# Kernel optimization log

Measured on AMD Instinct MI355X. Metric: run time of the kernel, lower is better.

Reference implementation:

```python
import jax, jax.numpy as jnp
import numpy as np


def _gcn_norm(edge_index, edge_weight, n_nodes):
    # PyG gcn_norm with add_self_loops=True, fill_value=1.0.
    row, col = edge_index[0], edge_index[1]
    loop = jnp.arange(n_nodes, dtype=edge_index.dtype)
    row = jnp.concatenate([row, loop])
    col = jnp.concatenate([col, loop])
    w = jnp.concatenate([edge_weight, jnp.ones((n_nodes,), edge_weight.dtype)])
    deg = jax.ops.segment_sum(w, col, num_segments=n_nodes)
    dinv = jnp.where(deg > 0, jax.lax.rsqrt(deg), 0.0)
    norm = dinv[row] * w * dinv[col]
    return row, col, norm


def _gcn_conv(x, row, col, norm, W, b, n_nodes):
    h = x @ W                                  # [N, F_out]
    msg = h[row] * norm[:, None]               # gather + scale, [E+N, F_out]
    out = jax.ops.segment_sum(msg, col, num_segments=n_nodes)
    return out + b


def setup_inputs() -> dict:
    key = jax.random.key(0)
    k = jax.random.split(key, 7)
    N, E, Fin, Fout = 50000, 1600000, 256, 128
    H = 2 * Fout
    x = jax.random.normal(k[0], (N, Fin), dtype=jnp.float32)
    edge_index = jax.random.randint(k[1], (2, E), 0, N, dtype=jnp.int64)
    edge_weight = jax.random.uniform(k[2], (E,), dtype=jnp.float32)
    # Glorot init as in PyG GCNConv (weight stored as [in, out] here)
    s1 = float(np.sqrt(6.0 / (Fin + H)))
    s2 = float(np.sqrt(6.0 / (H + Fout)))
    W1 = jax.random.uniform(k[3], (Fin, H), minval=-s1, maxval=s1, dtype=jnp.float32)
    b1 = jnp.zeros((H,), jnp.float32)
    W2 = jax.random.uniform(k[4], (H, Fout), minval=-s2, maxval=s2, dtype=jnp.float32)
    b2 = jnp.zeros((Fout,), jnp.float32)
    return {"x": x, "edge_index": edge_index, "edge_weight": edge_weight,
            "W1": W1, "b1": b1, "W2": W2, "b2": b2}


def reference(x, edge_index, edge_weight, W1, b1, W2, b2):
    n_nodes = x.shape[0]
    # cached=True: normalization computed once, reused by both layers
    row, col, norm = _gcn_norm(edge_index, edge_weight, n_nodes)
    h = _gcn_conv(x, row, col, norm, W1, b1, n_nodes)
    h = jax.nn.relu(h)
    out = _gcn_conv(h, row, col, norm, W2, b2, n_nodes)
    return out
```

## Files before the change

### kernel.cpp

```cpp
#include <hip/hip_runtime.h>

typedef __attribute__((ext_vector_type(8))) short  short8;
typedef __attribute__((ext_vector_type(4))) float  f32x4;
typedef __attribute__((ext_vector_type(4))) ushort us4;
typedef __attribute__((ext_vector_type(4))) uint   u32x4;
typedef __attribute__((ext_vector_type(2))) uint   u32x2;

__device__ __forceinline__ float bf2f(ushort u) {
    union { uint i; float f; } c; c.i = ((uint)u) << 16; return c.f;
}
__device__ __forceinline__ float bits2f(uint b) {
    union { uint i; float f; } c; c.i = b; return c.f;
}
__device__ __forceinline__ ushort f2bf(float f) {
    union { float f; uint i; } c; c.f = f;
    uint b = c.i + 0x7fffu + ((c.i >> 16) & 1u);
    return (ushort)(b >> 16);
}

#define CMAX  96
#define NBLK  256
#define NBMAX 1024

__global__ void k_histA(const int* __restrict__ col, int* __restrict__ counts,
                        int E, int NB) {
    __shared__ uint hist[NBMAX];
    for (int j = threadIdx.x; j < NB; j += 256) hist[j] = 0u;
    __syncthreads();
    for (int i = blockIdx.x * 256 + threadIdx.x; i < E; i += 256 * NBLK)
        atomicAdd(&hist[((uint)col[i]) >> 6], 1u);
    __syncthreads();
    for (int j = threadIdx.x; j < NB; j += 256)
        counts[j * NBLK + blockIdx.x] = (int)hist[j];
}

__global__ void k_scanB1(int* __restrict__ counts, int* __restrict__ btot) {
    __shared__ int s[256];
    int b = blockIdx.x, t = threadIdx.x;
    int v = counts[b * NBLK + t];
    s[t] = v; __syncthreads();
    for (int off = 1; off < 256; off <<= 1) {
        int x = (t >= off) ? s[t - off] : 0;
        __syncthreads();
        s[t] += x;
        __syncthreads();
    }
    counts[b * NBLK + t] = s[t] - v;
    if (t == 255) btot[b] = s[255];
}

__global__ void k_scanB2(const int* __restrict__ btot, int* __restrict__ bbase, int NB) {
    __shared__ int s[256];
    int t = threadIdx.x;
    int v[4]; int sum = 0;
    #pragma unroll
    for (int j = 0; j < 4; ++j) {
        int i = t * 4 + j;
        v[j] = (i < NB) ? btot[i] : 0;
        sum += v[j];
    }
    s[t] = sum; __syncthreads();
    for (int off = 1; off < 256; off <<= 1) {
        int x = (t >= off) ? s[t - off] : 0;
        __syncthreads();
        s[t] += x;
        __syncthreads();
    }
    int excl = s[t] - sum;
    #pragma unroll
    for (int j = 0; j < 4; ++j) {
        int i = t * 4 + j;
        if (i <= NB) bbase[i] = excl;
        excl += v[j];
    }
}

__global__ void k_binC(const int* __restrict__ row, const int* __restrict__ col,
                       const float* __restrict__ w,
                       const int* __restrict__ counts, const int* __restrict__ bbase,
                       unsigned long long* __restrict__ recs, int E, int NB) {
    __shared__ uint cur[NBMAX];
    for (int j = threadIdx.x; j < NB; j += 256)
        cur[j] = (uint)(bbase[j] + counts[j * NBLK + blockIdx.x]);
    __syncthreads();
    for (int i = blockIdx.x * 256 + threadIdx.x; i < E; i += 256 * NBLK) {
        int c = col[i], r = row[i];
        float wv = w[i];
        uint w16 = (uint)(wv * 65536.0f);
        if (w16 > 65535u) w16 = 65535u;
        uint b = ((uint)c) >> 6;
        uint pos = atomicAdd(&cur[b], 1u);
        recs[pos] = ((unsigned long long)(uint)c << 32)
                  | (unsigned long long)((w16 << 16) | (uint)(r & 0xffff));
    }
}

__global__ void k_binD(const unsigned long long* __restrict__ recs,
                       const int* __restrict__ bbase,
                       uint* __restrict__ edgesP, int* __restrict__ cntp,
                       float* __restrict__ dinv, int N, int NB) {
    __shared__ uint cnt[64], ws[64], cur2[64];
    int b = blockIdx.x, t = threadIdx.x;
    if (t < 64) { cnt[t] = 0u; ws[t] = 0u; cur2[t] = 0u; }
    __syncthreads();
    int lo = bbase[b], hi = bbase[b + 1];
    for (int i = lo + t; i < hi; i += 256) {
        unsigned long long rec = recs[i];
        uint cl = ((uint)(rec >> 32)) & 63u;
        atomicAdd(&cnt[cl], 1u);
        atomicAdd(&ws[cl], (uint)((rec >> 16) & 0xffffu));
    }
    __syncthreads();
    for (int i = lo + t; i < hi; i += 256) {
        unsigned long long rec = recs[i];
        uint cg = (uint)(rec >> 32);
        uint slot = atomicAdd(&cur2[cg & 63u], 1u);
        if (slot < CMAX) edgesP[(size_t)cg * CMAX + slot] = (uint)rec;
    }
    __syncthreads();
    if (t < 64) {
        int node = b * 64 + t;
        if (node < N) {
            uint c0 = cnt[t];
            if (c0 > CMAX) c0 = CMAX;
            int cp = (int)((c0 + 3u) & ~3u);
            for (int j = (int)c0; j < cp; ++j)
                edgesP[(size_t)node * CMAX + j] = 0u;
            float deg = 1.0f + (float)ws[t] * (1.0f / 65536.0f);
            dinv[node] = rsqrtf(deg);
            cntp[node] = cp;
        }
    }
}

__global__ void k_splitT(const float* __restrict__ W, ushort* __restrict__ Th,
                         ushort* __restrict__ Tl, int K, int N) {
    int i = blockIdx.x * 256 + threadIdx.x;
    if (i < K * N) {
        int k = i / N, n = i - k * N;
        float v = W[i];
        ushort hi = f2bf(v);
        ushort lo = f2bf(v - bf2f(hi));
        Th[(size_t)n * K + k] = hi;
        Tl[(size_t)n * K + k] = lo;
    }
}

#define LDA 40

__global__ __launch_bounds__(256)
void k_gemm3(const float* __restrict__ A, const ushort* __restrict__ BTh,
             const ushort* __restrict__ BTl, ushort* __restrict__ Cpan,
             const float* __restrict__ dinv, int M, int Nc, int K) {
    __shared__ __align__(16) ushort As[2][128][LDA];
    __shared__ __align__(16) ushort Bs[2][128][LDA];

    const int t    = threadIdx.x;
    const int lane = t & 63;
    const int wid  = t >> 6;
    const int wm   = wid >> 1;
    const int wn   = wid & 1;
    const int ml   = lane & 15;
    const int kq   = lane >> 4;
    const int bm   = blockIdx.y * 128;
    const int bn   = blockIdx.x * 128;

    f32x4 acc[4][4];
    #pragma unroll
    for (int mt = 0; mt < 4; ++mt)
        #pragma unroll
        for (int nt = 0; nt < 4; ++nt) acc[mt][nt] = (f32x4){0.f, 0.f, 0.f, 0.f};

    for (int k0 = 0; k0 < K; k0 += 32) {
        #pragma unroll
        for (int it = 0; it < 4; ++it) {
            int idx = (t + it * 256) * 4;
            int r  = idx >> 5;
            int kk = idx & 31;
            int grow = bm + r;
            f32x4 v = (f32x4){0.f, 0.f, 0.f, 0.f};
            if (grow < M) v = *(const f32x4*)&A[(size_t)grow * K + k0 + kk];
            us4 hi, lo;
            #pragma unroll
            for (int j = 0; j < 4; ++j) {
                ushort h = f2bf(v[j]);
                hi[j] = h;
                lo[j] = f2bf(v[j] - bf2f(h));
            }
            *(us4*)&As[0][r][kk] = hi;
            *(us4*)&As[1][r][kk] = lo;
        }
        #pragma unroll
        for (int it = 0; it < 2; ++it) {
            int idx = (t + it * 256) * 8;
            int n  = idx >> 5;
            int kk = idx & 31;
            u32x4 vh = *(const u32x4*)&BTh[(size_t)(bn + n) * K + k0 + kk];
            *(u32x4*)&Bs[0][n][kk] = vh;
            u32x4 vl = *(const u32x4*)&BTl[(size_t)(bn + n) * K + k0 + kk];
            *(u32x4*)&Bs[1][n][kk] = vl;
        }
        __syncthreads();

        short8 a[4][2], b[4][2];
        #pragma unroll
        for (int mt = 0; mt < 4; ++mt) {
            a[mt][0] = *(const short8*)&As[0][wm * 64 + mt * 16 + ml][kq * 8];
            a[mt][1] = *(const short8*)&As[1][wm * 64 + mt * 16 + ml][kq * 8];
        }
        #pragma unroll
        for (int nt = 0; nt < 4; ++nt) {
            b[nt][0] = *(const short8*)&Bs[0][wn * 64 + nt * 16 + ml][kq * 8];
            b[nt][1] = *(const short8*)&Bs[1][wn * 64 + nt * 16 + ml][kq * 8];
        }
        #pragma unroll
        for (int mt = 0; mt < 4; ++mt)
            #pragma unroll
            for (int nt = 0; nt < 4; ++nt) {
                acc[mt][nt] = __builtin_amdgcn_mfma_f32_16x16x32_bf16(a[mt][0], b[nt][0], acc[mt][nt], 0, 0, 0);
                acc[mt][nt] = __builtin_amdgcn_mfma_f32_16x16x32_bf16(a[mt][0], b[nt][1], acc[mt][nt], 0, 0, 0);
                acc[mt][nt] = __builtin_amdgcn_mfma_f32_16x16x32_bf16(a[mt][1], b[nt][0], acc[mt][nt], 0, 0, 0);
            }
        __syncthreads();
    }

    #pragma unroll
    for (int mt = 0; mt < 4; ++mt) {
        int rbase = bm + wm * 64 + mt * 16 + kq * 4;
        #pragma unroll
        for (int nt = 0; nt < 4; ++nt) {
            int colg = bn + wn * 64 + nt * 16 + ml;
            size_t pbase = (size_t)(colg >> 5) * M * 32 + (colg & 31);
            #pragma unroll
            for (int r = 0; r < 4; ++r) {
                int rr = rbase + r;
                if (rr < M) Cpan[pbase + (size_t)rr * 32] = f2bf(acc[mt][nt][r] * dinv[rr]);
            }
        }
    }
}

#define NODES_PER_BLK 32

template <bool RELU>
__device__ __forceinline__
void aggr_body(const int* __restrict__ cntp, const uint* __restrict__ edges,
               const ushort* __restrict__ hpan, const float* __restrict__ dinv,
               const float* __restrict__ bias, float* __restrict__ out,
               int F, int npan, int N) {
    const int bid  = blockIdx.x;
    const int p    = bid % npan;
    const int wave = threadIdx.x >> 6;
    const int lane = threadIdx.x & 63;
    const int g    = lane >> 3;
    const int c    = lane & 7;
    const int node = (bid / npan) * NODES_PER_BLK + wave * 8 + g;
    const int fbase = p * 32 + c * 4;

    const ushort* hp = hpan + (size_t)p * N * 32 + c * 4;

    int beg = 0, end = 0;
    if (node < N) { beg = node * CMAX; end = beg + cntp[node]; }

    float a0 = 0.f, a1 = 0.f, a2 = 0.f, a3 = 0.f;
    int e = beg;
    u32x4 pk4 = (u32x4){0u, 0u, 0u, 0u};
    if (e < end) pk4 = *(const u32x4*)&edges[e];
    while (__any(e < end)) {
        u32x4 cur = pk4;
        int e2 = e + 4;
        if (e2 < end) pk4 = *(const u32x4*)&edges[e2];
        if (e < end) {
            #pragma unroll
            for (int j = 0; j < 4; ++j) {
                uint pk = cur[j];
                float nv = (float)(pk >> 16);
                int r = (int)(pk & 0xffffu);
                u32x2 hv = *(const u32x2*)(hp + (size_t)r * 32);
                a0 += nv * bits2f(hv[0] << 16);
                a1 += nv * bits2f(hv[0] & 0xffff0000u);
                a2 += nv * bits2f(hv[1] << 16);
                a3 += nv * bits2f(hv[1] & 0xffff0000u);
            }
        }
        e = e2;
    }

    if (node < N) {
        float dc = dinv[node];
        float sc = dc * (1.0f / 65536.0f);
        u32x2 hs = *(const u32x2*)(hp + (size_t)node * 32);
        f32x4 bv = *(const f32x4*)&bias[fbase];
        f32x4 v;
        v[0] = fmaf(sc, a0, fmaf(dc, bits2f(hs[0] << 16),         bv[0]));
        v[1] = fmaf(sc, a1, fmaf(dc, bits2f(hs[0] & 0xffff0000u), bv[1]));
        v[2] = fmaf(sc, a2, fmaf(dc, bits2f(hs[1] << 16),         bv[2]));
        v[3] = fmaf(sc, a3, fmaf(dc, bits2f(hs[1] & 0xffff0000u), bv[3]));
        if (RELU) {
            v[0] = fmaxf(v[0], 0.f); v[1] = fmaxf(v[1], 0.f);
            v[2] = fmaxf(v[2], 0.f); v[3] = fmaxf(v[3], 0.f);
        }
        *(f32x4*)&out[(size_t)node * F + fbase] = v;
    }
}

__global__ __launch_bounds__(256)
void k_aggr1(const int* __restrict__ cntp, const uint* __restrict__ edges,
             const ushort* __restrict__ hpan, const float* __restrict__ dinv,
             const float* __restrict__ bias, float* __restrict__ out,
             int F, int npan, int N) {
    aggr_body<true>(cntp, edges, hpan, dinv, bias, out, F, npan, N);
}

__global__ __launch_bounds__(256)
void k_aggr2(const int* __restrict__ cntp, const uint* __restrict__ edges,
             const ushort* __restrict__ hpan, const float* __restrict__ dinv,
             const float* __restrict__ bias, float* __restrict__ out,
             int F, int npan, int N) {
    aggr_body<false>(cntp, edges, hpan, dinv, bias, out, F, npan, N);
}


static inline char* bump(char*& p, size_t bytes) {
    char* r = p;
    p += (bytes + 255) & ~(size_t)255;
    return r;
}

extern "C" void kernel_launch(void* const* d_in, const int* in_sizes, int n_in,
                              void* d_out, int out_size, void* d_ws, size_t ws_size,
                              hipStream_t stream) {
    const float* x  = (const float*)d_in[0];
    const int*   ei = (const int*)d_in[1];
    const float* ew = (const float*)d_in[2];
    const float* W1 = (const float*)d_in[3];
    const float* b1 = (const float*)d_in[4];
    const float* W2 = (const float*)d_in[5];
    const float* b2 = (const float*)d_in[6];
    float* out = (float*)d_out;

    const int E    = in_sizes[2];
    const int H    = in_sizes[4];
    const int Fout = in_sizes[6];
    const int Fin  = in_sizes[3] / H;
    const int N    = in_sizes[0] / Fin;
    const int NB   = (N + 63) >> 6;

    const int* row = ei;
    const int* col = ei + E;

    char* p = (char*)d_ws;
    float*  dinv   = (float*)bump(p, (size_t)N * 4);
    int*    cntp   = (int*)bump(p, (size_t)N * 4);
    uint*   edgesP = (uint*)bump(p, (size_t)N * CMAX * 4);
    int*    counts = (int*)bump(p, (size_t)NBMAX * NBLK * 4);
    int*    btot   = (int*)bump(p, (size_t)NBMAX * 4);
    int*    bbase  = (int*)bump(p, (size_t)(NBMAX + 1) * 4);
    ushort* WT1h   = (ushort*)bump(p, (size_t)Fin * H * 2);
    ushort* WT1l   = (ushort*)bump(p, (size_t)Fin * H * 2);
    ushort* WT2h   = (ushort*)bump(p, (size_t)H * Fout * 2);
    ushort* WT2l   = (ushort*)bump(p, (size_t)H * Fout * 2);
    ushort* h1     = (ushort*)bump(p, (size_t)N * H * 2);
    float*  a1     = (float*)bump(p, (size_t)N * H * 4);
    ushort* h2     = (ushort*)bump(p, (size_t)N * Fout * 2);

    unsigned long long* recs = (unsigned long long*)a1;

    k_splitT<<<(Fin * H + 255) / 256, 256, 0, stream>>>(W1, WT1h, WT1l, Fin, H);
    k_splitT<<<(H * Fout + 255) / 256, 256, 0, stream>>>(W2, WT2h, WT2l, H, Fout);

    k_histA<<<NBLK, 256, 0, stream>>>(col, counts, E, NB);
    k_scanB1<<<NB, 256, 0, stream>>>(counts, btot);
    k_scanB2<<<1, 256, 0, stream>>>(btot, bbase, NB);
    k_binC<<<NBLK, 256, 0, stream>>>(row, col, ew, counts, bbase, recs, E, NB);
    k_binD<<<NB, 256, 0, stream>>>(recs, bbase, edgesP, cntp, dinv, N, NB);

    const int chunks = (N + NODES_PER_BLK - 1) / NODES_PER_BLK;

    k_gemm3<<<dim3(H / 128, (N + 127) / 128), 256, 0, stream>>>(x, WT1h, WT1l, h1, dinv, N, H, Fin);
    k_aggr1<<<chunks * (H / 32), 256, 0, stream>>>(cntp, edgesP, h1, dinv, b1, a1, H, H / 32, N);

    k_gemm3<<<dim3(Fout / 128, (N + 127) / 128), 256, 0, stream>>>(a1, WT2h, WT2l, h2, dinv, N, Fout, H);
    k_aggr2<<<chunks * (Fout / 32), 256, 0, stream>>>(cntp, edgesP, h2, dinv, b2, out, Fout, Fout / 32, N);
}
```

Baseline: 419.6 us.

## Overlap graph binning with layer-1 GEMM and switch to compact CSR with precomputed norms

Fuses the histogram and weight-split kernels into one launch. The edge binning and degree stages now share launches with slices of the layer-1 GEMM so that graph preprocessing overlaps matrix work, which is possible because the GEMM no longer scales its output by dinv. Edges move from a fixed CMAX=96 slot-per-node layout to a compact CSR with per-bin prefix sums, and each edge stores its full normalized weight in bf16, so aggregation no longer applies dinv. This adds an extra scan and pass, removes the degree truncation at CMAX, and lowers precision of the edge norm to bf16.

```diff
diff --git a/kernel.cpp b/kernel.cpp
--- a/kernel.cpp
+++ b/kernel.cpp
@@ -5,6 +5,7 @@
 typedef __attribute__((ext_vector_type(4))) ushort us4;
 typedef __attribute__((ext_vector_type(4))) uint   u32x4;
 typedef __attribute__((ext_vector_type(2))) uint   u32x2;
+typedef unsigned long long ull;
 
 __device__ __forceinline__ float bf2f(ushort u) {
     union { uint i; float f; } c; c.i = ((uint)u) << 16; return c.f;
@@ -18,13 +19,12 @@
     return (ushort)(b >> 16);
 }
 
-#define CMAX  96
 #define NBLK  256
 #define NBMAX 1024
 
-__global__ void k_histA(const int* __restrict__ col, int* __restrict__ counts,
-                        int E, int NB) {
-    __shared__ uint hist[NBMAX];
+__device__ __forceinline__
+void histA_body(const int* __restrict__ col, int* __restrict__ counts,
+                int E, int NB, uint* hist) {
     for (int j = threadIdx.x; j < NB; j += 256) hist[j] = 0u;
     __syncthreads();
     for (int i = blockIdx.x * 256 + threadIdx.x; i < E; i += 256 * NBLK)
@@ -32,6 +32,102 @@
     __syncthreads();
     for (int j = threadIdx.x; j < NB; j += 256)
         counts[j * NBLK + blockIdx.x] = (int)hist[j];
+}
+
+__device__ __forceinline__
+void binC_body(const int* __restrict__ row, const int* __restrict__ col,
+               const float* __restrict__ w,
+               const int* __restrict__ counts, const int* __restrict__ bbase,
+               ull* __restrict__ recs, int E, int NB, uint* cur) {
+    for (int j = threadIdx.x; j < NB; j += 256)
+        cur[j] = (uint)(bbase[j] + counts[j * NBLK + blockIdx.x]);
+    __syncthreads();
+    for (int i = blockIdx.x * 256 + threadIdx.x; i < E; i += 256 * NBLK) {
+        int c = col[i], r = row[i];
+        float wv = w[i];
+        uint w16 = (uint)(wv * 65536.0f);
+        if (w16 > 65535u) w16 = 65535u;
+        uint pos = atomicAdd(&cur[((uint)c) >> 6], 1u);
+        recs[pos] = ((ull)(uint)c << 32) | (ull)((w16 << 16) | (uint)(r & 0xffff));
+    }
+}
+
+__device__ __forceinline__
+void binDa_body(const ull* __restrict__ recs, const int* __restrict__ bbase,
+                int* __restrict__ cntp, float* __restrict__ dinv,
+                int* __restrict__ btotP, int N,
+                uint* cnt, uint* ws, uint* red) {
+    int b = blockIdx.x, t = threadIdx.x;
+    if (t < 64) { cnt[t] = 0u; ws[t] = 0u; }
+    __syncthreads();
+    int lo = bbase[b], hi = bbase[b + 1];
+    for (int i = lo + t; i < hi; i += 256) {
+        ull rec = recs[i];
+        atomicAdd(&cnt[((uint)(rec >> 32)) & 63u], 1u);
+        atomicAdd(&ws[((uint)(rec >> 32)) & 63u], (uint)((rec >> 16) & 0xffffu));
+    }
+    __syncthreads();
+    uint cp = 0;
+    if (t < 64) {
+        int node = b * 64 + t;
+        if (node < N) {
+            cp = (cnt[t] + 3u) & ~3u;
+            cntp[node] = (int)cp;
+            dinv[node] = rsqrtf(1.0f + (float)ws[t] * (1.0f / 65536.0f));
+        }
+        red[t] = cp;
+    }
+    __syncthreads();
+    if (t < 32) red[t] += red[t + 32];
+    __syncthreads();
+    if (t < 16) red[t] += red[t + 16];
+    __syncthreads();
+    if (t < 8) red[t] += red[t + 8];
+    __syncthreads();
+    if (t < 4) red[t] += red[t + 4];
+    __syncthreads();
+    if (t == 0) btotP[b] = (int)(red[0] + red[1] + red[2] + red[3]);
+}
+
+__device__ __forceinline__
+void binDb_body(const ull* __restrict__ recs, const int* __restrict__ bbase,
+                const int* __restrict__ bbaseP, const int* __restrict__ cntp,
+                const float* __restrict__ dinv, int* __restrict__ rowptr,
+                uint* __restrict__ edgesP, int N,
+                uint* arr, uint* curN, uint* rbs) {
+    int b = blockIdx.x, t = threadIdx.x;
+    int node = b * 64 + t;
+    uint cp = 0;
+    if (t < 64 && node < N) cp = (uint)cntp[node];
+    if (t < 64) arr[t] = cp;
+    __syncthreads();
+    for (int off = 1; off < 64; off <<= 1) {
+        uint x = (t < 64 && t >= off) ? arr[t - off] : 0u;
+        __syncthreads();
+        if (t < 64) arr[t] += x;
+        __syncthreads();
+    }
+    if (t < 64) {
+        uint rb = (uint)bbaseP[b] + arr[t] - cp;
+        rbs[t] = rb; curN[t] = rb;
+        if (node < N) rowptr[node] = (int)rb;
+    }
+    __syncthreads();
+    int lo = bbase[b], hi = bbase[b + 1];
+    for (int i = lo + t; i < hi; i += 256) {
+        ull rec = recs[i];
+        uint c   = (uint)(rec >> 32);
+        uint r   = (uint)rec & 0xffffu;
+        uint w16 = ((uint)rec >> 16) & 0xffffu;
+        float nv = dinv[r] * ((float)w16 * (1.0f / 65536.0f)) * dinv[c];
+        uint slot = atomicAdd(&curN[c & 63u], 1u);
+        edgesP[slot] = r | ((uint)f2bf(nv) << 16);
+    }
+    __syncthreads();
+    if (t < 64 && node < N) {
+        uint e1 = rbs[t] + cp;
+        for (uint j = curN[t]; j < e1; ++j) edgesP[j] = 0u;
+    }
 }
 
 __global__ void k_scanB1(int* __restrict__ counts, int* __restrict__ btot) {
@@ -75,67 +171,9 @@
     }
 }
 
-__global__ void k_binC(const int* __restrict__ row, const int* __restrict__ col,
-                       const float* __restrict__ w,
-                       const int* __restrict__ counts, const int* __restrict__ bbase,
-                       unsigned long long* __restrict__ recs, int E, int NB) {
-    __shared__ uint cur[NBMAX];
-    for (int j = threadIdx.x; j < NB; j += 256)
-        cur[j] = (uint)(bbase[j] + counts[j * NBLK + blockIdx.x]);
-    __syncthreads();
-    for (int i = blockIdx.x * 256 + threadIdx.x; i < E; i += 256 * NBLK) {
-        int c = col[i], r = row[i];
-        float wv = w[i];
-        uint w16 = (uint)(wv * 65536.0f);
-        if (w16 > 65535u) w16 = 65535u;
-        uint b = ((uint)c) >> 6;
-        uint pos = atomicAdd(&cur[b], 1u);
-        recs[pos] = ((unsigned long long)(uint)c << 32)
-                  | (unsigned long long)((w16 << 16) | (uint)(r & 0xffff));
-    }
-}
-
-__global__ void k_binD(const unsigned long long* __restrict__ recs,
-                       const int* __restrict__ bbase,
-                       uint* __restrict__ edgesP, int* __restrict__ cntp,
-                       float* __restrict__ dinv, int N, int NB) {
-    __shared__ uint cnt[64], ws[64], cur2[64];
-    int b = blockIdx.x, t = threadIdx.x;
-    if (t < 64) { cnt[t] = 0u; ws[t] = 0u; cur2[t] = 0u; }
-    __syncthreads();
-    int lo = bbase[b], hi = bbase[b + 1];
-    for (int i = lo + t; i < hi; i += 256) {
-        unsigned long long rec = recs[i];
-        uint cl = ((uint)(rec >> 32)) & 63u;
-        atomicAdd(&cnt[cl], 1u);
-        atomicAdd(&ws[cl], (uint)((rec >> 16) & 0xffffu));
-    }
-    __syncthreads();
-    for (int i = lo + t; i < hi; i += 256) {
-        unsigned long long rec = recs[i];
-        uint cg = (uint)(rec >> 32);
-        uint slot = atomicAdd(&cur2[cg & 63u], 1u);
-        if (slot < CMAX) edgesP[(size_t)cg * CMAX + slot] = (uint)rec;
-    }
-    __syncthreads();
-    if (t < 64) {
-        int node = b * 64 + t;
-        if (node < N) {
-            uint c0 = cnt[t];
-            if (c0 > CMAX) c0 = CMAX;
-            int cp = (int)((c0 + 3u) & ~3u);
-            for (int j = (int)c0; j < cp; ++j)
-                edgesP[(size_t)node * CMAX + j] = 0u;
-            float deg = 1.0f + (float)ws[t] * (1.0f / 65536.0f);
-            dinv[node] = rsqrtf(deg);
-            cntp[node] = cp;
-        }
-    }
-}
-
-__global__ void k_splitT(const float* __restrict__ W, ushort* __restrict__ Th,
-                         ushort* __restrict__ Tl, int K, int N) {
-    int i = blockIdx.x * 256 + threadIdx.x;
+__device__ __forceinline__
+void splitT_body(const float* __restrict__ W, ushort* __restrict__ Th,
+                 ushort* __restrict__ Tl, int K, int N, int i) {
     if (i < K * N) {
         int k = i / N, n = i - k * N;
         float v = W[i];
@@ -148,13 +186,11 @@
 
 #define LDA 40
 
-__global__ __launch_bounds__(256)
-void k_gemm3(const float* __restrict__ A, const ushort* __restrict__ BTh,
-             const ushort* __restrict__ BTl, ushort* __restrict__ Cpan,
-             const float* __restrict__ dinv, int M, int Nc, int K) {
-    __shared__ __align__(16) ushort As[2][128][LDA];
-    __shared__ __align__(16) ushort Bs[2][128][LDA];
-
+__device__ __forceinline__
+void gemm3_body(const float* __restrict__ A, const ushort* __restrict__ BTh,
+                const ushort* __restrict__ BTl, ushort* __restrict__ Cpan,
+                int M, int Nc, int K, int bm, int bn,
+                ushort (*As)[128][LDA], ushort (*Bs)[128][LDA]) {
     const int t    = threadIdx.x;
     const int lane = t & 63;
     const int wid  = t >> 6;
@@ -162,8 +198,6 @@
     const int wn   = wid & 1;
     const int ml   = lane & 15;
     const int kq   = lane >> 4;
-    const int bm   = blockIdx.y * 128;
-    const int bn   = blockIdx.x * 128;
 
     f32x4 acc[4][4];
     #pragma unroll
@@ -234,17 +268,97 @@
             #pragma unroll
             for (int r = 0; r < 4; ++r) {
                 int rr = rbase + r;
-                if (rr < M) Cpan[pbase + (size_t)rr * 32] = f2bf(acc[mt][nt][r] * dinv[rr]);
+                if (rr < M) Cpan[pbase + (size_t)rr * 32] = f2bf(acc[mt][nt][r]);
             }
         }
     }
 }
 
+__global__ __launch_bounds__(256)
+void k_gemm3(const float* __restrict__ A, const ushort* __restrict__ BTh,
+             const ushort* __restrict__ BTl, ushort* __restrict__ Cpan,
+             int M, int Nc, int K) {
+    __shared__ __align__(16) ushort As[2][128][LDA];
+    __shared__ __align__(16) ushort Bs[2][128][LDA];
+    gemm3_body(A, BTh, BTl, Cpan, M, Nc, K, blockIdx.y * 128, blockIdx.x * 128, As, Bs);
+}
+
+__global__ __launch_bounds__(256)
+void k_fusedA(const int* __restrict__ col, int* __restrict__ counts, int E, int NB,
+              const float* __restrict__ W1, ushort* __restrict__ WT1h, ushort* __restrict__ WT1l,
+              int Fin, int H,
+              const float* __restrict__ W2, ushort* __restrict__ WT2h, ushort* __restrict__ WT2l,
+              int Fout, int sp1) {
+    __shared__ uint hist[NBMAX];
+    int bid = (int)blockIdx.x;
+    if (bid < NBLK) { histA_body(col, counts, E, NB, hist); return; }
+    if (bid < NBLK + sp1) { splitT_body(W1, WT1h, WT1l, Fin, H, (bid - NBLK) * 256 + (int)threadIdx.x); return; }
+    splitT_body(W2, WT2h, WT2l, H, Fout, (bid - NBLK - sp1) * 256 + (int)threadIdx.x);
+}
+
+__global__ __launch_bounds__(256)
+void k_fusedB1(const int* __restrict__ row, const int* __restrict__ col,
+               const float* __restrict__ w, const int* __restrict__ counts,
+               const int* __restrict__ bbase, ull* __restrict__ recs, int E, int NB,
+               const float* __restrict__ A, const ushort* __restrict__ BTh,
+               const ushort* __restrict__ BTl, ushort* __restrict__ Cpan,
+               int M, int Nc, int K, int t0) {
+    __shared__ __align__(16) ushort As[2][128][LDA];
+    __shared__ __align__(16) ushort Bs[2][128][LDA];
+    int bid = (int)blockIdx.x;
+    if (bid < NBLK) { binC_body(row, col, w, counts, bbase, recs, E, NB, (uint*)&As[0][0][0]); return; }
+    int tile = t0 + bid - NBLK;
+    int nbn = Nc >> 7;
+    gemm3_body(A, BTh, BTl, Cpan, M, Nc, K, (tile / nbn) * 128, (tile % nbn) * 128, As, Bs);
+}
+
+__global__ __launch_bounds__(256)
+void k_fusedB2(const ull* __restrict__ recs, const int* __restrict__ bbase,
+               int* __restrict__ cntp, float* __restrict__ dinv, int* __restrict__ btotP,
+               int N, int NB,
+               const float* __restrict__ A, const ushort* __restrict__ BTh,
+               const ushort* __restrict__ BTl, ushort* __restrict__ Cpan,
+               int M, int Nc, int K, int t0) {
+    __shared__ __align__(16) ushort As[2][128][LDA];
+    __shared__ __align__(16) ushort Bs[2][128][LDA];
+    int bid = (int)blockIdx.x;
+    if (bid < NB) {
+        uint* l = (uint*)&As[0][0][0];
+        binDa_body(recs, bbase, cntp, dinv, btotP, N, l, l + 64, l + 128);
+        return;
+    }
+    int tile = t0 + bid - NB;
+    int nbn = Nc >> 7;
+    gemm3_body(A, BTh, BTl, Cpan, M, Nc, K, (tile / nbn) * 128, (tile % nbn) * 128, As, Bs);
+}
+
+__global__ __launch_bounds__(256)
+void k_fusedB3(const ull* __restrict__ recs, const int* __restrict__ bbase,
+               const int* __restrict__ bbaseP, const int* __restrict__ cntp,
+               const float* __restrict__ dinv, int* __restrict__ rowptr,
+               uint* __restrict__ edgesP, int N, int NB,
+               const float* __restrict__ A, const ushort* __restrict__ BTh,
+               const ushort* __restrict__ BTl, ushort* __restrict__ Cpan,
+               int M, int Nc, int K, int t0) {
+    __shared__ __align__(16) ushort As[2][128][LDA];
+    __shared__ __align__(16) ushort Bs[2][128][LDA];
+    int bid = (int)blockIdx.x;
+    if (bid < NB) {
+        uint* l = (uint*)&As[0][0][0];
+        binDb_body(recs, bbase, bbaseP, cntp, dinv, rowptr, edgesP, N, l, l + 64, l + 128);
+        return;
+    }
+    int tile = t0 + bid - NB;
+    int nbn = Nc >> 7;
+    gemm3_body(A, BTh, BTl, Cpan, M, Nc, K, (tile / nbn) * 128, (tile % nbn) * 128, As, Bs);
+}
+
 #define NODES_PER_BLK 32
 
 template <bool RELU>
 __device__ __forceinline__
-void aggr_body(const int* __restrict__ cntp, const uint* __restrict__ edges,
+void aggr_body(const int* __restrict__ rowptr, const int* __restrict__ cntp,
+               const uint* __restrict__ edges,
                const ushort* __restrict__ hpan, const float* __restrict__ dinv,
                const float* __restrict__ bias, float* __restrict__ out,
                int F, int npan, int N) {
@@ -260,7 +374,7 @@
     const ushort* hp = hpan + (size_t)p * N * 32 + c * 4;
 
     int beg = 0, end = 0;
-    if (node < N) { beg = node * CMAX; end = beg + cntp[node]; }
+    if (node < N) { beg = rowptr[node]; end = beg + cntp[node]; }
 
     float a0 = 0.f, a1 = 0.f, a2 = 0.f, a3 = 0.f;
     int e = beg;
@@ -274,7 +388,7 @@
             #pragma unroll
             for (int j = 0; j < 4; ++j) {
                 uint pk = cur[j];
-                float nv = (float)(pk >> 16);
+                float nv = bits2f(pk & 0xffff0000u);
                 int r = (int)(pk & 0xffffu);
                 u32x2 hv = *(const u32x2*)(hp + (size_t)r * 32);
                 a0 += nv * bits2f(hv[0] << 16);
@@ -287,15 +401,15 @@
     }
 
     if (node < N) {
-        float dc = dinv[node];
-        float sc = dc * (1.0f / 65536.0f);
+        float di = dinv[node];
+        float d2 = di * di;
         u32x2 hs = *(const u32x2*)(hp + (size_t)node * 32);
         f32x4 bv = *(const f32x4*)&bias[fbase];
         f32x4 v;
-        v[0] = fmaf(sc, a0, fmaf(dc, bits2f(hs[0] << 16),         bv[0]));
-        v[1] = fmaf(sc, a1, fmaf(dc, bits2f(hs[0] & 0xffff0000u), bv[1]));
-        v[2] = fmaf(sc, a2, fmaf(dc, bits2f(hs[1] << 16),         bv[2]));
-        v[3] = fmaf(sc, a3, fmaf(dc, bits2f(hs[1] & 0xffff0000u), bv[3]));
+        v[0] = a0 + d2 * bits2f(hs[0] << 16)         + bv[0];
+        v[1] = a1 + d2 * bits2f(hs[0] & 0xffff0000u) + bv[1];
+        v[2] = a2 + d2 * bits2f(hs[1] << 16)         + bv[2];
+        v[3] = a3 + d2 * bits2f(hs[1] & 0xffff0000u) + bv[3];
         if (RELU) {
             v[0] = fmaxf(v[0], 0.f); v[1] = fmaxf(v[1], 0.f);
             v[2] = fmaxf(v[2], 0.f); v[3] = fmaxf(v[3], 0.f);
@@ -305,19 +419,19 @@
 }
 
 __global__ __launch_bounds__(256)
-void k_aggr1(const int* __restrict__ cntp, const uint* __restrict__ edges,
-             const ushort* __restrict__ hpan, const float* __restrict__ dinv,
-             const float* __restrict__ bias, float* __restrict__ out,
-             int F, int npan, int N) {
-    aggr_body<true>(cntp, edges, hpan, dinv, bias, out, F, npan, N);
-}
-
-__global__ __launch_bounds__(256)
-void k_aggr2(const int* __restrict__ cntp, const uint* __restrict__ edges,
-             const ushort* __restrict__ hpan, const float* __restrict__ dinv,
-             const float* __restrict__ bias, float* __restrict__ out,
-             int F, int npan, int N) {
-    aggr_body<false>(cntp, edges, hpan, dinv, bias, out, F, npan, N);
+void k_aggr1(const int* __restrict__ rowptr, const int* __restrict__ cntp,
+             const uint* __restrict__ edges, const ushort* __restrict__ hpan,
+             const float* __restrict__ dinv, const float* __restrict__ bias,
+             float* __restrict__ out, int F, int npan, int N) {
+    aggr_body<true>(rowptr, cntp, edges, hpan, dinv, bias, out, F, npan, N);
+}
+
+__global__ __launch_bounds__(256)
+void k_aggr2(const int* __restrict__ rowptr, const int* __restrict__ cntp,
+             const uint* __restrict__ edges, const ushort* __restrict__ hpan,
+             const float* __restrict__ dinv, const float* __restrict__ bias,
+             float* __restrict__ out, int F, int npan, int N) {
+    aggr_body<false>(rowptr, cntp, edges, hpan, dinv, bias, out, F, npan, N);
 }
 
 
@@ -352,10 +466,13 @@
     char* p = (char*)d_ws;
     float*  dinv   = (float*)bump(p, (size_t)N * 4);
     int*    cntp   = (int*)bump(p, (size_t)N * 4);
-    uint*   edgesP = (uint*)bump(p, (size_t)N * CMAX * 4);
+    int*    rowptr = (int*)bump(p, (size_t)N * 4);
+    uint*   edgesP = (uint*)bump(p, ((size_t)E + 4 * N + 256) * 4);
     int*    counts = (int*)bump(p, (size_t)NBMAX * NBLK * 4);
     int*    btot   = (int*)bump(p, (size_t)NBMAX * 4);
     int*    bbase  = (int*)bump(p, (size_t)(NBMAX + 1) * 4);
+    int*    btotP  = (int*)bump(p, (size_t)NBMAX * 4);
+    int*    bbaseP = (int*)bump(p, (size_t)(NBMAX + 1) * 4);
     ushort* WT1h   = (ushort*)bump(p, (size_t)Fin * H * 2);
     ushort* WT1l   = (ushort*)bump(p, (size_t)Fin * H * 2);
     ushort* WT2h   = (ushort*)bump(p, (size_t)H * Fout * 2);
@@ -364,22 +481,33 @@
     float*  a1     = (float*)bump(p, (size_t)N * H * 4);
     ushort* h2     = (ushort*)bump(p, (size_t)N * Fout * 2);
 
-    unsigned long long* recs = (unsigned long long*)a1;
-
-    k_splitT<<<(Fin * H + 255) / 256, 256, 0, stream>>>(W1, WT1h, WT1l, Fin, H);
-    k_splitT<<<(H * Fout + 255) / 256, 256, 0, stream>>>(W2, WT2h, WT2l, H, Fout);
-
-    k_histA<<<NBLK, 256, 0, stream>>>(col, counts, E, NB);
+    ull* recs = (ull*)a1;
+
+    const int sp1 = (Fin * H + 255) / 256;
+    const int sp2 = (H * Fout + 255) / 256;
+    const int gb1 = (H / 128) * ((N + 127) / 128);
+    int T1 = gb1 < 280 ? gb1 : 280;
+    int T2 = gb1 < 480 ? gb1 : 480;
+    if (T2 < T1) T2 = T1;
+
+    k_fusedA<<<NBLK + sp1 + sp2, 256, 0, stream>>>(col, counts, E, NB,
+                                                   W1, WT1h, WT1l, Fin, H,
+                                                   W2, WT2h, WT2l, Fout, sp1);
     k_scanB1<<<NB, 256, 0, stream>>>(counts, btot);
     k_scanB2<<<1, 256, 0, stream>>>(btot, bbase, NB);
-    k_binC<<<NBLK, 256, 0, stream>>>(row, col, ew, counts, bbase, recs, E, NB);
-    k_binD<<<NB, 256, 0, stream>>>(recs, bbase, edgesP, cntp, dinv, N, NB);
+    k_fusedB1<<<NBLK + T1, 256, 0, stream>>>(row, col, ew, counts, bbase, recs, E, NB,
+                                             x, WT1h, WT1l, h1, N, H, Fin, 0);
+    k_fusedB2<<<NB + (T2 - T1), 256, 0, stream>>>(recs, bbase, cntp, dinv, btotP, N, NB,
+                                                  x, WT1h, WT1l, h1, N, H, Fin, T1);
+    k_scanB2<<<1, 256, 0, stream>>>(btotP, bbaseP, NB);
+    k_fusedB3<<<NB + (gb1 - T2), 256, 0, stream>>>(recs, bbase, bbaseP, cntp, dinv,
+                                                   rowptr, edgesP, N, NB,
+                                                   x, WT1h, WT1l, h1, N, H, Fin, T2);
 
     const int chunks = (N + NODES_PER_BLK - 1) / NODES_PER_BLK;
 
-    k_gemm3<<<dim3(H / 128, (N + 127) / 128), 256, 0, stream>>>(x, WT1h, WT1l, h1, dinv, N, H, Fin);
-    k_aggr1<<<chunks * (H / 32), 256, 0, stream>>>(cntp, edgesP, h1, dinv, b1, a1, H, H / 32, N);
-
-    k_gemm3<<<dim3(Fout / 128, (N + 127) / 128), 256, 0, stream>>>(a1, WT2h, WT2l, h2, dinv, N, Fout, H);
-    k_aggr2<<<chunks * (Fout / 32), 256, 0, stream>>>(cntp, edgesP, h2, dinv, b2, out, Fout, Fout / 32, N);
-}
+    k_aggr1<<<chunks * (H / 32), 256, 0, stream>>>(rowptr, cntp, edgesP, h1, dinv, b1, a1, H, H / 32, N);
+
+    k_gemm3<<<dim3(Fout / 128, (N + 127) / 128), 256, 0, stream>>>(a1, WT2h, WT2l, h2, N, Fout, H);
+    k_aggr2<<<chunks * (Fout / 32), 256, 0, stream>>>(rowptr, cntp, edgesP, h2, dinv, b2, out, Fout, Fout / 32, N);
+}
```

Measured after the change: 421.0 us. About the same (+0.3%).
